# Performance work log

Hardware: AMD Instinct MI355X
Metric: run time of the kernel (lower is better)

Reference implementation:

```python
import jax, jax.numpy as jnp
import numpy as np

N, E, D, H = 100000, 600000, 128, 512  # nodes, edges, latent_dim, 4*latent_dim


def setup_inputs() -> dict:
    key = jax.random.key(0)
    ks = jax.random.split(key, 9)
    s = 0.05
    return {
        "z": jax.random.normal(ks[0], (N, D), dtype=jnp.float32),
        "edge_index": jax.random.randint(ks[1], (2, E), 0, N, dtype=jnp.int64),
        "Wg": jax.random.normal(ks[2], (D, D), dtype=jnp.float32) * s,
        "Ws": jax.random.normal(ks[3], (D, D), dtype=jnp.float32) * s,
        "bg": jnp.zeros((D,), dtype=jnp.float32),
        "W1": jax.random.normal(ks[4], (D, H), dtype=jnp.float32) * s,
        "b1": jnp.zeros((H,), dtype=jnp.float32),
        "W2": jax.random.normal(ks[5], (H, H), dtype=jnp.float32) * s,
        "b2": jnp.zeros((H,), dtype=jnp.float32),
        "W3": jax.random.normal(ks[6], (H, D), dtype=jnp.float32) * s,
        "b3": jnp.zeros((D,), dtype=jnp.float32),
    }


def reference(z, edge_index, Wg, Ws, bg, W1, b1, W2, b2, W3, b3):
    src, dst = edge_index[0], edge_index[1]
    n = z.shape[0]
    # GNN: gather neighbor features along edges, mean-aggregate at dst
    msgs = z[src]                                   # (E, D) gather
    agg = jax.ops.segment_sum(msgs, dst, num_segments=n)  # (N, D) scatter-add
    deg = jax.ops.segment_sum(jnp.ones((src.shape[0],), z.dtype), dst, num_segments=n)
    agg = agg / jnp.maximum(deg, 1.0)[:, None]      # mean aggregation
    h = jax.nn.relu(agg @ Wg + z @ Ws + bg)          # (N, D) graph conv output
    # MLP: Linear -> Tanh -> Linear -> Tanh -> Linear
    h = jnp.tanh(h @ W1 + b1)
    h = jnp.tanh(h @ W2 + b2)
    return h @ W3 + b3                               # dz/dt: (N, D)
```

## Files before the change

kernel.cpp:

```cpp
#include <hip/hip_runtime.h>
#include <hip/hip_fp16.h>


typedef _Float16 f16;
typedef __attribute__((ext_vector_type(4))) _Float16 f16x4;
typedef __attribute__((ext_vector_type(8))) _Float16 f16x8;
typedef __attribute__((ext_vector_type(4))) float f32x4;

__device__ __forceinline__ void async_load16(const void* g, void* lds) {
  __builtin_amdgcn_global_load_lds(
      (const __attribute__((address_space(1))) void*)g,
      (__attribute__((address_space(3))) void*)lds, 16, 0, 0);
}

__device__ __forceinline__ float fast_tanh(float x) {
  float a = fabsf(x);
  float e = __expf(-2.0f * a);
  float r = (1.0f - e) * __builtin_amdgcn_rcpf(1.0f + e);
  return copysignf(r, x);
}

__global__ __launch_bounds__(256) void zero_kernel(int* __restrict__ p, int n) {
  int i = blockIdx.x * 256 + threadIdx.x;
  int stride = gridDim.x * 256;
  for (; i < n; i += stride) p[i] = 0;
}

__global__ __launch_bounds__(256) void deg_count(const int* __restrict__ dst,
                                                 int* __restrict__ degi, int E) {
  int e = blockIdx.x * 256 + threadIdx.x;
  if (e < E) atomicAdd(&degi[dst[e]], 1);
}

__global__ __launch_bounds__(256) void scan_partial(const int* __restrict__ degi,
                                                    int* __restrict__ bsum, int N) {
  __shared__ int lds[256];
  int b = blockIdx.x, t = threadIdx.x;
  int s = 0;
#pragma unroll
  for (int j = 0; j < 4; ++j) {
    int idx = b * 1024 + t * 4 + j;
    if (idx < N) s += degi[idx];
  }
  lds[t] = s;
  __syncthreads();
  for (int off = 128; off > 0; off >>= 1) {
    if (t < off) lds[t] += lds[t + off];
    __syncthreads();
  }
  if (t == 0) bsum[b] = lds[0];
}

__global__ void scan_bsums(const int* __restrict__ bsum, int* __restrict__ boff,
                           int* __restrict__ row_start, int nb, int N) {
  if (threadIdx.x == 0 && blockIdx.x == 0) {
    int acc = 0;
    for (int i = 0; i < nb; ++i) { boff[i] = acc; acc += bsum[i]; }
    row_start[N] = acc;
  }
}

__global__ __launch_bounds__(256) void scan_final(
    const int* __restrict__ degi, const int* __restrict__ boff,
    int* __restrict__ row_start, int* __restrict__ cursor, int N) {
  __shared__ int lds[256];
  int b = blockIdx.x, t = threadIdx.x;
  int base = b * 1024;
  int v[4];
  int s = 0;
#pragma unroll
  for (int j = 0; j < 4; ++j) {
    int idx = base + t * 4 + j;
    v[j] = (idx < N) ? degi[idx] : 0;
    s += v[j];
  }
  lds[t] = s;
  __syncthreads();
  for (int off = 1; off < 256; off <<= 1) {
    int x = lds[t];
    int y = (t >= off) ? lds[t - off] : 0;
    __syncthreads();
    lds[t] = x + y;
    __syncthreads();
  }
  int pre = boff[b] + lds[t] - s;
#pragma unroll
  for (int j = 0; j < 4; ++j) {
    int idx = base + t * 4 + j;
    if (idx < N) { row_start[idx] = pre; cursor[idx] = pre; pre += v[j]; }
  }
}

__global__ __launch_bounds__(256) void fill_adj(const int* __restrict__ src,
                                                const int* __restrict__ dst,
                                                int* __restrict__ cursor,
                                                int* __restrict__ adj, int E) {
  int e = blockIdx.x * 256 + threadIdx.x;
  if (e >= E) return;
  int p = atomicAdd(&cursor[dst[e]], 1);
  adj[p] = src[e];
}

__global__ __launch_bounds__(256) void cast_z16(const float* __restrict__ z,
                                                f16* __restrict__ z16, int n4) {
  int i = blockIdx.x * 256 + threadIdx.x;
  int stride = gridDim.x * 256;
  for (; i < n4; i += stride) {
    float4 v = *(const float4*)(z + 4 * (long long)i);
    f16x4 c;
    c[0] = (f16)v.x; c[1] = (f16)v.y; c[2] = (f16)v.z; c[3] = (f16)v.w;
    *(f16x4*)(z16 + 4 * (long long)i) = c;
  }
}

__global__ __launch_bounds__(256) void gather_xcat(
    const f16* __restrict__ z16, const int* __restrict__ row_start,
    const int* __restrict__ adj, f16* __restrict__ Xc, int N) {
  int node = (blockIdx.x * 256 + threadIdx.x) >> 5;
  if (node >= N) return;
  int lane = threadIdx.x & 31;
  int beg = row_start[node], end = row_start[node + 1];
  float a0 = 0, a1 = 0, a2 = 0, a3 = 0;
  float b0 = 0, b1 = 0, b2 = 0, b3 = 0;
  float c0 = 0, c1 = 0, c2 = 0, c3 = 0;
  float d0 = 0, d1 = 0, d2 = 0, d3 = 0;
  int i = beg;
  for (; i + 4 <= end; i += 4) {
    int n0 = adj[i], n1 = adj[i + 1], n2 = adj[i + 2], n3 = adj[i + 3];
    f16x4 v0 = *(const f16x4*)(z16 + (long long)n0 * 128 + 4 * lane);
    f16x4 v1 = *(const f16x4*)(z16 + (long long)n1 * 128 + 4 * lane);
    f16x4 v2 = *(const f16x4*)(z16 + (long long)n2 * 128 + 4 * lane);
    f16x4 v3 = *(const f16x4*)(z16 + (long long)n3 * 128 + 4 * lane);
    a0 += (float)v0[0]; a1 += (float)v0[1]; a2 += (float)v0[2]; a3 += (float)v0[3];
    b0 += (float)v1[0]; b1 += (float)v1[1]; b2 += (float)v1[2]; b3 += (float)v1[3];
    c0 += (float)v2[0]; c1 += (float)v2[1]; c2 += (float)v2[2]; c3 += (float)v2[3];
    d0 += (float)v3[0]; d1 += (float)v3[1]; d2 += (float)v3[2]; d3 += (float)v3[3];
  }
  for (; i < end; ++i) {
    f16x4 v = *(const f16x4*)(z16 + (long long)adj[i] * 128 + 4 * lane);
    a0 += (float)v[0]; a1 += (float)v[1]; a2 += (float)v[2]; a3 += (float)v[3];
  }
  a0 += b0 + c0 + d0; a1 += b1 + c1 + d1;
  a2 += b2 + c2 + d2; a3 += b3 + c3 + d3;
  int dg = end - beg;
  float inv = 1.0f / (float)(dg > 1 ? dg : 1);
  long long o = (long long)node * 256;
  f16x4 m;
  m[0] = (f16)(a0 * inv); m[1] = (f16)(a1 * inv);
  m[2] = (f16)(a2 * inv); m[3] = (f16)(a3 * inv);
  *(f16x4*)(Xc + o + 4 * lane) = m;
  *(f16x4*)(Xc + o + 128 + 4 * lane) =
      *(const f16x4*)(z16 + (long long)node * 128 + 4 * lane);
}

__global__ __launch_bounds__(256) void prep_weights(
    const float* __restrict__ Wg, const float* __restrict__ Ws,
    const float* __restrict__ W1, const float* __restrict__ W2,
    const float* __restrict__ W3, f16* __restrict__ wgs, f16* __restrict__ wt1,
    f16* __restrict__ wt2, f16* __restrict__ wt3) {
  int i = blockIdx.x * 256 + threadIdx.x;
  int stride = gridDim.x * 256;
  for (; i < 425984; i += stride) {
    if (i < 32768) {
      int n = i >> 8, k = i & 255;
      wgs[i] = (f16)((k < 128) ? Wg[k * 128 + n] : Ws[(k - 128) * 128 + n]);
    } else if (i < 98304) {
      int j = i - 32768, c = j >> 7, k = j & 127;
      wt1[j] = (f16)W1[k * 512 + c];
    } else if (i < 360448) {
      int j = i - 98304, c = j >> 9, k = j & 511;
      wt2[j] = (f16)W2[k * 512 + c];
    } else {
      int j = i - 360448, c = j >> 9, k = j & 511;
      wt3[j] = (f16)W3[k * 128 + c];
    }
  }
}

template <int K, int NOUT, int WM, int WN, int MI, int ACT, bool OUTF32>
__global__ __launch_bounds__(WM * WN * 64) void gemm_r(
    const f16* __restrict__ X, const f16* __restrict__ Wt,
    const float* __restrict__ bias, void* __restrict__ OutV, int M) {
  constexpr int NJ = 4;
  constexpr int BM = WM * MI * 16;
  constexpr int BN = WN * NJ * 16;
  constexpr int NTHR = WM * WN * 64;
  constexpr int CA = (BM * 128) / (NTHR * 16);
  constexpr int CB = (BN * 128) / (NTHR * 16);
  __shared__ __align__(16) f16 As[BM * 64];
  __shared__ __align__(16) f16 Bs[BN * 64];

  const int tid = threadIdx.x;
  const int wid = tid >> 6, lane = tid & 63;
  const int wm = wid / WN, wn = wid % WN;
  const int lr = lane & 15, lq = lane >> 4;
  const int rxor = lr & 7;
  const long long m0 = (long long)blockIdx.x * BM;
  const int n0 = blockIdx.y * BN;

  const f16* Ag = X + m0 * K;
  const f16* Bg = Wt + (long long)n0 * K;

  long long aOff[CA], bOff[CB];
#pragma unroll
  for (int c = 0; c < CA; ++c) {
    int f = c * NTHR + tid;
    int row = f >> 3, ss = (f & 7) ^ (row & 7);
    aOff[c] = (long long)row * K + ss * 8;
  }
#pragma unroll
  for (int c = 0; c < CB; ++c) {
    int f = c * NTHR + tid;
    int row = f >> 3, ss = (f & 7) ^ (row & 7);
    bOff[c] = (long long)row * K + ss * 8;
  }

  f32x4 acc[MI][NJ];
#pragma unroll
  for (int i = 0; i < MI; ++i)
#pragma unroll
    for (int j = 0; j < NJ; ++j)
#pragma unroll
      for (int r = 0; r < 4; ++r) acc[i][j][r] = 0.0f;

#pragma unroll 1
  for (int k0 = 0; k0 < K; k0 += 64) {
#pragma unroll
    for (int c = 0; c < CA; ++c)
      async_load16(Ag + aOff[c] + k0, (char*)As + c * NTHR * 16 + wid * 1024);
#pragma unroll
    for (int c = 0; c < CB; ++c)
      async_load16(Bg + bOff[c] + k0, (char*)Bs + c * NTHR * 16 + wid * 1024);
    __syncthreads();
#pragma unroll
    for (int kk = 0; kk < 64; kk += 32) {
      const int co = (((kk >> 3) + lq) ^ rxor) * 16;
      f16x8 a[MI], b[NJ];
#pragma unroll
      for (int i = 0; i < MI; ++i)
        a[i] = *reinterpret_cast<const f16x8*>(
            (const char*)As + (wm * MI * 16 + i * 16 + lr) * 128 + co);
#pragma unroll
      for (int j = 0; j < NJ; ++j)
        b[j] = *reinterpret_cast<const f16x8*>(
            (const char*)Bs + (wn * NJ * 16 + j * 16 + lr) * 128 + co);
#pragma unroll
      for (int i = 0; i < MI; ++i)
#pragma unroll
        for (int j = 0; j < NJ; ++j)
          acc[i][j] = __builtin_amdgcn_mfma_f32_16x16x32_f16(a[i], b[j], acc[i][j], 0, 0, 0);
    }
    __syncthreads();
  }

#pragma unroll
  for (int i = 0; i < MI; ++i) {
#pragma unroll
    for (int j = 0; j < NJ; ++j) {
      int col = n0 + wn * NJ * 16 + j * 16 + lr;
      float bv = bias[col];
#pragma unroll
      for (int r = 0; r < 4; ++r) {
        long long row = m0 + wm * MI * 16 + i * 16 + lq * 4 + r;
        if (row < M) {
          float v = acc[i][j][r] + bv;
          if (ACT == 1) v = fmaxf(v, 0.0f);
          else if (ACT == 2) v = fast_tanh(v);
          if constexpr (OUTF32)
            ((float*)OutV)[row * NOUT + col] = v;
          else
            ((f16*)OutV)[row * NOUT + col] = (f16)v;
        }
      }
    }
  }
}

extern "C" void kernel_launch(void* const* d_in, const int* in_sizes, int n_in,
                              void* d_out, int out_size, void* d_ws, size_t ws_size,
                              hipStream_t stream) {
  const float* z  = (const float*)d_in[0];
  const int*   ei = (const int*)d_in[1];
  const float* Wg = (const float*)d_in[2];
  const float* Ws = (const float*)d_in[3];
  const float* bg = (const float*)d_in[4];
  const float* W1 = (const float*)d_in[5];
  const float* b1 = (const float*)d_in[6];
  const float* W2 = (const float*)d_in[7];
  const float* b2 = (const float*)d_in[8];
  const float* W3 = (const float*)d_in[9];
  const float* b3 = (const float*)d_in[10];

  const int Nn = in_sizes[0] / 128;
  const int E  = in_sizes[1] / 2;
  const int* src = ei;
  const int* dst = ei + E;
  const int nb = (Nn + 1023) / 1024;
  const int gm128 = (Nn + 127) / 128;
  const long long Mpad = (long long)gm128 * 128;

  char* base = (char*)d_ws;
  const size_t XCB = (size_t)Mpad * 256 * 2;
  const size_t H1B = (size_t)Mpad * 128 * 2;
  const size_t H3B = (size_t)Mpad * 512 * 2;
  f16* Xc = (f16*)(base);
  f16* h1 = (f16*)(base + XCB);
  f16* h3 = (f16*)(base);
  size_t off = XCB + H1B;
  auto alloc = [&](size_t b) -> void* {
    void* p = base + off;
    off += (b + 255) & ~(size_t)255;
    return p;
  };
  int* degi      = (int*)alloc((size_t)Nn * 4);
  int* row_start = (int*)alloc((size_t)(Nn + 1) * 4);
  int* cursor    = (int*)alloc((size_t)Nn * 4);
  int* adj       = (int*)alloc((size_t)E * 4);
  int* bsum      = (int*)alloc((size_t)nb * 4);
  int* boff      = (int*)alloc((size_t)nb * 4);
  f16* z16       = (f16*)alloc((size_t)Nn * 128 * 2);
  off = H3B;
  f16* h2  = (f16*)alloc((size_t)Mpad * 512 * 2);
  f16* wgs = (f16*)alloc((size_t)128 * 256 * 2);
  f16* wt1 = (f16*)alloc((size_t)512 * 128 * 2);
  f16* wt2 = (f16*)alloc((size_t)512 * 512 * 2);
  f16* wt3 = (f16*)alloc((size_t)128 * 512 * 2);

  zero_kernel<<<(Nn + 255) / 256, 256, 0, stream>>>(degi, Nn);
  deg_count<<<(E + 255) / 256, 256, 0, stream>>>(dst, degi, E);
  scan_partial<<<nb, 256, 0, stream>>>(degi, bsum, Nn);
  scan_bsums<<<1, 64, 0, stream>>>(bsum, boff, row_start, nb, Nn);
  scan_final<<<nb, 256, 0, stream>>>(degi, boff, row_start, cursor, Nn);
  fill_adj<<<(E + 255) / 256, 256, 0, stream>>>(src, dst, cursor, adj, E);

  prep_weights<<<416, 256, 0, stream>>>(Wg, Ws, W1, W2, W3, wgs, wt1, wt2, wt3);
  cast_z16<<<2048, 256, 0, stream>>>(z, z16, Nn * 32);

  {
    long long tot = (long long)Nn * 32;
    gather_xcat<<<(int)((tot + 255) / 256), 256, 0, stream>>>(z16, row_start, adj, Xc, Nn);
  }

  gemm_r<256, 128, 2, 2, 4, 1, false><<<dim3(gm128, 1), 256, 0, stream>>>(Xc, wgs, bg, (void*)h1, Nn);
  gemm_r<128, 512, 2, 4, 4, 2, false><<<dim3(gm128, 2), 512, 0, stream>>>(h1, wt1, b1, (void*)h2, Nn);
  gemm_r<512, 512, 2, 4, 4, 2, false><<<dim3(gm128, 2), 512, 0, stream>>>(h2, wt2, b2, (void*)h3, Nn);
  gemm_r<512, 128, 2, 2, 4, 0, true><<<dim3(gm128, 1), 256, 0, stream>>>(h3, wt3, b3, d_out, Nn);
}
```

Before: 337.7 us.

## Add double-buffered async-LDS GEMM for MLP layers and restructure gather

Adds a new GEMM kernel that double-buffers K-tiles of 32 in LDS through async global-to-LDS loads, with explicit waitcnt and barrier, and uses it for the two 512-wide hidden layers. The gather kernel now issues eight predicated neighbor loads up front, so typical low-degree nodes load with more memory parallelism. The self-feature copy into the concatenated buffer moves into the cast kernel. The aim is to hide global latency in the large GEMMs and cut gather latency, at the cost of extra LDS use and wasted loads for nodes with fewer than eight neighbours.

```diff
diff --git a/kernel.cpp b/kernel.cpp
--- a/kernel.cpp
+++ b/kernel.cpp
@@ -12,6 +12,13 @@
       (const __attribute__((address_space(1))) void*)g,
       (__attribute__((address_space(3))) void*)lds, 16, 0, 0);
 }
+
+#define VMBAR()                                         \
+  do {                                                  \
+    asm volatile("s_waitcnt vmcnt(0)" ::: "memory");    \
+    __builtin_amdgcn_s_barrier();                       \
+    __builtin_amdgcn_sched_barrier(0);                  \
+  } while (0)
 
 __device__ __forceinline__ float fast_tanh(float x) {
   float a = fabsf(x);
@@ -102,7 +109,8 @@
 }
 
 __global__ __launch_bounds__(256) void cast_z16(const float* __restrict__ z,
-                                                f16* __restrict__ z16, int n4) {
+                                                f16* __restrict__ z16,
+                                                f16* __restrict__ Xc, int n4) {
   int i = blockIdx.x * 256 + threadIdx.x;
   int stride = gridDim.x * 256;
   for (; i < n4; i += stride) {
@@ -110,6 +118,8 @@
     f16x4 c;
     c[0] = (f16)v.x; c[1] = (f16)v.y; c[2] = (f16)v.z; c[3] = (f16)v.w;
     *(f16x4*)(z16 + 4 * (long long)i) = c;
+    int node = i >> 5, sl = i & 31;
+    *(f16x4*)(Xc + (long long)node * 256 + 128 + 4 * sl) = c;
   }
 }
 
@@ -121,27 +131,39 @@
   int lane = threadIdx.x & 31;
   int beg = row_start[node], end = row_start[node + 1];
   float a0 = 0, a1 = 0, a2 = 0, a3 = 0;
-  float b0 = 0, b1 = 0, b2 = 0, b3 = 0;
-  float c0 = 0, c1 = 0, c2 = 0, c3 = 0;
-  float d0 = 0, d1 = 0, d2 = 0, d3 = 0;
-  int i = beg;
-  for (; i + 4 <= end; i += 4) {
-    int n0 = adj[i], n1 = adj[i + 1], n2 = adj[i + 2], n3 = adj[i + 3];
-    f16x4 v0 = *(const f16x4*)(z16 + (long long)n0 * 128 + 4 * lane);
-    f16x4 v1 = *(const f16x4*)(z16 + (long long)n1 * 128 + 4 * lane);
-    f16x4 v2 = *(const f16x4*)(z16 + (long long)n2 * 128 + 4 * lane);
-    f16x4 v3 = *(const f16x4*)(z16 + (long long)n3 * 128 + 4 * lane);
-    a0 += (float)v0[0]; a1 += (float)v0[1]; a2 += (float)v0[2]; a3 += (float)v0[3];
-    b0 += (float)v1[0]; b1 += (float)v1[1]; b2 += (float)v1[2]; b3 += (float)v1[3];
-    c0 += (float)v2[0]; c1 += (float)v2[1]; c2 += (float)v2[2]; c3 += (float)v2[3];
-    d0 += (float)v3[0]; d1 += (float)v3[1]; d2 += (float)v3[2]; d3 += (float)v3[3];
-  }
-  for (; i < end; ++i) {
-    f16x4 v = *(const f16x4*)(z16 + (long long)adj[i] * 128 + 4 * lane);
-    a0 += (float)v[0]; a1 += (float)v[1]; a2 += (float)v[2]; a3 += (float)v[3];
-  }
-  a0 += b0 + c0 + d0; a1 += b1 + c1 + d1;
-  a2 += b2 + c2 + d2; a3 += b3 + c3 + d3;
+#pragma unroll
+  for (int j = 0; j < 8; ++j) {
+    int idx = beg + j;
+    bool vld = idx < end;
+    int nb = vld ? adj[idx] : node;
+    f16x4 x = *(const f16x4*)(z16 + (long long)nb * 128 + 4 * lane);
+    float w = vld ? 1.0f : 0.0f;
+    a0 += w * (float)x[0]; a1 += w * (float)x[1];
+    a2 += w * (float)x[2]; a3 += w * (float)x[3];
+  }
+  int i = beg + 8;
+  if (i < end) {
+    float b0 = 0, b1 = 0, b2 = 0, b3 = 0;
+    float c0 = 0, c1 = 0, c2 = 0, c3 = 0;
+    float d0 = 0, d1 = 0, d2 = 0, d3 = 0;
+    for (; i + 4 <= end; i += 4) {
+      int n0 = adj[i], n1 = adj[i + 1], n2 = adj[i + 2], n3 = adj[i + 3];
+      f16x4 v0 = *(const f16x4*)(z16 + (long long)n0 * 128 + 4 * lane);
+      f16x4 v1 = *(const f16x4*)(z16 + (long long)n1 * 128 + 4 * lane);
+      f16x4 v2 = *(const f16x4*)(z16 + (long long)n2 * 128 + 4 * lane);
+      f16x4 v3 = *(const f16x4*)(z16 + (long long)n3 * 128 + 4 * lane);
+      a0 += (float)v0[0]; a1 += (float)v0[1]; a2 += (float)v0[2]; a3 += (float)v0[3];
+      b0 += (float)v1[0]; b1 += (float)v1[1]; b2 += (float)v1[2]; b3 += (float)v1[3];
+      c0 += (float)v2[0]; c1 += (float)v2[1]; c2 += (float)v2[2]; c3 += (float)v2[3];
+      d0 += (float)v3[0]; d1 += (float)v3[1]; d2 += (float)v3[2]; d3 += (float)v3[3];
+    }
+    for (; i < end; ++i) {
+      f16x4 v = *(const f16x4*)(z16 + (long long)adj[i] * 128 + 4 * lane);
+      a0 += (float)v[0]; a1 += (float)v[1]; a2 += (float)v[2]; a3 += (float)v[3];
+    }
+    a0 += b0 + c0 + d0; a1 += b1 + c1 + d1;
+    a2 += b2 + c2 + d2; a3 += b3 + c3 + d3;
+  }
   int dg = end - beg;
   float inv = 1.0f / (float)(dg > 1 ? dg : 1);
   long long o = (long long)node * 256;
@@ -149,8 +171,6 @@
   m[0] = (f16)(a0 * inv); m[1] = (f16)(a1 * inv);
   m[2] = (f16)(a2 * inv); m[3] = (f16)(a3 * inv);
   *(f16x4*)(Xc + o + 4 * lane) = m;
-  *(f16x4*)(Xc + o + 128 + 4 * lane) =
-      *(const f16x4*)(z16 + (long long)node * 128 + 4 * lane);
 }
 
 __global__ __launch_bounds__(256) void prep_weights(
@@ -276,6 +296,113 @@
   }
 }
 
+template <int K, int NOUT, int WM, int WN, int ACT, bool OUTF32>
+__global__ __launch_bounds__(WM * WN * 64) void gemm_d(
+    const f16* __restrict__ X, const f16* __restrict__ Wt,
+    const float* __restrict__ bias, void* __restrict__ OutV, int M) {
+  constexpr int BM = WM * 64;
+  constexpr int BN = WN * 64;
+  constexpr int NTHR = WM * WN * 64;
+  constexpr int CA = (BM * 4) / NTHR;
+  constexpr int CB = (BN * 4) / NTHR;
+  constexpr int NT = K / 32;
+  __shared__ __align__(16) f16 A0[BM * 32], A1[BM * 32];
+  __shared__ __align__(16) f16 B0[BN * 32], B1[BN * 32];
+
+  const int tid = threadIdx.x;
+  const int wid = tid >> 6, lane = tid & 63;
+  const int wm = wid / WN, wn = wid % WN;
+  const int lr = lane & 15, lq = lane >> 4;
+  const long long m0 = (long long)blockIdx.x * BM;
+  const int n0 = blockIdx.y * BN;
+
+  const f16* Ag = X + m0 * K;
+  const f16* Bg = Wt + (long long)n0 * K;
+
+  long long aOff[CA], bOff[CB];
+#pragma unroll
+  for (int c = 0; c < CA; ++c) {
+    int f = c * NTHR + tid;
+    int row = f >> 2, ss = (f & 3) ^ (row & 3);
+    aOff[c] = (long long)row * K + ss * 8;
+  }
+#pragma unroll
+  for (int c = 0; c < CB; ++c) {
+    int f = c * NTHR + tid;
+    int row = f >> 2, ss = (f & 3) ^ (row & 3);
+    bOff[c] = (long long)row * K + ss * 8;
+  }
+
+  f32x4 acc[4][4];
+#pragma unroll
+  for (int i = 0; i < 4; ++i)
+#pragma unroll
+    for (int j = 0; j < 4; ++j)
+#pragma unroll
+      for (int r = 0; r < 4; ++r) acc[i][j][r] = 0.0f;
+
+  auto STAGE = [&](f16* dA, f16* dB, int k0) {
+#pragma unroll
+    for (int c = 0; c < CA; ++c)
+      async_load16(Ag + aOff[c] + k0, (char*)dA + (c * NTHR + wid * 64) * 16);
+#pragma unroll
+    for (int c = 0; c < CB; ++c)
+      async_load16(Bg + bOff[c] + k0, (char*)dB + (c * NTHR + wid * 64) * 16);
+  };
+
+  const int co = ((lq ^ (lr & 3)) * 16);
+  auto COMPUTE = [&](const f16* sA, const f16* sB) {
+    f16x8 a[4], b[4];
+#pragma unroll
+    for (int i = 0; i < 4; ++i)
+      a[i] = *reinterpret_cast<const f16x8*>(
+          (const char*)sA + (wm * 64 + i * 16 + lr) * 64 + co);
+#pragma unroll
+    for (int j = 0; j < 4; ++j)
+      b[j] = *reinterpret_cast<const f16x8*>(
+          (const char*)sB + (wn * 64 + j * 16 + lr) * 64 + co);
+#pragma unroll
+    for (int i = 0; i < 4; ++i)
+#pragma unroll
+      for (int j = 0; j < 4; ++j)
+        acc[i][j] = __builtin_amdgcn_mfma_f32_16x16x32_f16(a[i], b[j], acc[i][j], 0, 0, 0);
+  };
+
+  STAGE(A0, B0, 0);
+  VMBAR();
+#pragma unroll 1
+  for (int t = 0; t < NT; t += 2) {
+    STAGE(A1, B1, (t + 1) * 32);
+    COMPUTE(A0, B0);
+    VMBAR();
+    if (t + 2 < NT) STAGE(A0, B0, (t + 2) * 32);
+    COMPUTE(A1, B1);
+    if (t + 2 < NT) VMBAR();
+  }
+
+#pragma unroll
+  for (int i = 0; i < 4; ++i) {
+#pragma unroll
+    for (int j = 0; j < 4; ++j) {
+      int col = n0 + wn * 64 + j * 16 + lr;
+      float bv = bias[col];
+#pragma unroll
+      for (int r = 0; r < 4; ++r) {
+        long long row = m0 + wm * 64 + i * 16 + lq * 4 + r;
+        if (row < M) {
+          float v = acc[i][j][r] + bv;
+          if (ACT == 1) v = fmaxf(v, 0.0f);
+          else if (ACT == 2) v = fast_tanh(v);
+          if constexpr (OUTF32)
+            ((float*)OutV)[row * NOUT + col] = v;
+          else
+            ((f16*)OutV)[row * NOUT + col] = (f16)v;
+        }
+      }
+    }
+  }
+}
+
 extern "C" void kernel_launch(void* const* d_in, const int* in_sizes, int n_in,
                               void* d_out, int out_size, void* d_ws, size_t ws_size,
                               hipStream_t stream) {
@@ -315,7 +442,7 @@
   int* degi      = (int*)alloc((size_t)Nn * 4);
   int* row_start = (int*)alloc((size_t)(Nn + 1) * 4);
   int* cursor    = (int*)alloc((size_t)Nn * 4);
-  int* adj       = (int*)alloc((size_t)E * 4);
+  int* adj       = (int*)alloc((size_t)(E + 8) * 4);
   int* bsum      = (int*)alloc((size_t)nb * 4);
   int* boff      = (int*)alloc((size_t)nb * 4);
   f16* z16       = (f16*)alloc((size_t)Nn * 128 * 2);
@@ -334,7 +461,7 @@
   fill_adj<<<(E + 255) / 256, 256, 0, stream>>>(src, dst, cursor, adj, E);
 
   prep_weights<<<416, 256, 0, stream>>>(Wg, Ws, W1, W2, W3, wgs, wt1, wt2, wt3);
-  cast_z16<<<2048, 256, 0, stream>>>(z, z16, Nn * 32);
+  cast_z16<<<2048, 256, 0, stream>>>(z, z16, Xc, Nn * 32);
 
   {
     long long tot = (long long)Nn * 32;
@@ -342,7 +469,7 @@
   }
 
   gemm_r<256, 128, 2, 2, 4, 1, false><<<dim3(gm128, 1), 256, 0, stream>>>(Xc, wgs, bg, (void*)h1, Nn);
-  gemm_r<128, 512, 2, 4, 4, 2, false><<<dim3(gm128, 2), 512, 0, stream>>>(h1, wt1, b1, (void*)h2, Nn);
-  gemm_r<512, 512, 2, 4, 4, 2, false><<<dim3(gm128, 2), 512, 0, stream>>>(h2, wt2, b2, (void*)h3, Nn);
+  gemm_d<128, 512, 2, 4, 2, false><<<dim3(gm128, 2), 512, 0, stream>>>(h1, wt1, b1, (void*)h2, Nn);
+  gemm_d<512, 512, 2, 4, 2, false><<<dim3(gm128, 2), 512, 0, stream>>>(h2, wt2, b2, (void*)h3, Nn);
   gemm_r<512, 128, 2, 2, 4, 0, true><<<dim3(gm128, 1), 256, 0, stream>>>(h3, wt3, b3, d_out, Nn);
 }
```

Measured after the change: 344.6 us. +2.0%, slower.
